# Performance work log

Measured on AMD Instinct MI355X. Metric: run time of the kernel, lower is better.

Reference implementation:

```python
import jax, jax.numpy as jnp
import numpy as np

B, S, C = 8, 512, 1024
H = 16
R = 32            # lora_rank
LORA_ALPHA = 1.0  # lora scaling (alpha=1)
HID = C           # mlp_ratio = 1


def setup_inputs() -> dict:
    key = jax.random.key(0)
    ks = jax.random.split(key, 20)
    g = lambda k, shp, s=0.02: jax.random.normal(k, shp, dtype=jnp.float32) * s
    inp = {
        "x": jax.random.normal(ks[0], (B, S, C), dtype=jnp.float32),
        "mask": jax.random.randint(ks[1], (B, 3 * S), 0, 2).astype(bool),
        # qkv: Linear(dim, 3*dim, bias=False), stored [in, out]
        "qkv_w": g(ks[2], (C, 3 * C)),
        "qkv_la": g(ks[3], (C, R)),
        "qkv_lb": g(ks[4], (R, 3 * C)),
        "proj_w": g(ks[5], (C, C)),
        "proj_b": jnp.zeros((C,), jnp.float32),
        "proj_la": g(ks[6], (C, R)),
        "proj_lb": g(ks[7], (R, C)),
        "fc1_w": g(ks[8], (C, HID)),
        "fc1_b": jnp.zeros((HID,), jnp.float32),
        "fc1_la": g(ks[9], (C, R)),
        "fc1_lb": g(ks[10], (R, HID)),
        "fc2_w": g(ks[11], (HID, C)),
        "fc2_b": jnp.zeros((C,), jnp.float32),
        "fc2_la": g(ks[12], (C, R)),
        "fc2_lb": g(ks[13], (R, C)),
    }
    return inp


def reference(x, mask, qkv_w, qkv_la, qkv_lb, proj_w, proj_b, proj_la, proj_lb,
              fc1_w, fc1_b, fc1_la, fc1_lb, fc2_w, fc2_b, fc2_la, fc2_lb):
    # cross_modality='a', mask_modality='a' (constants)
    b, s, c = x.shape
    hd = c // H
    scale = hd ** (-0.5)

    # fused QKV + LoRA low-rank update
    qkv = x @ qkv_w + ((x @ qkv_la) @ qkv_lb) * LORA_ALPHA      # [B,S,3C]
    qkv = qkv.reshape(b, s, 3, H, hd).transpose(2, 0, 3, 1, 4)  # [3,B,H,S,hd]
    q, k, v = qkv[0] * scale, qkv[1], qkv[2]

    # fp32 QK^T, modality 'a' mask slice, fill -inf, softmax, NaN->0
    attn = jnp.einsum('bhqd,bhkd->bhqk',
                      q.astype(jnp.float32), k.astype(jnp.float32))
    m = mask[:, :s]                                             # 'a' slice
    attn = jnp.where(m[:, None, None, :], attn, -jnp.inf)
    attn = jax.nn.softmax(attn, axis=-1).astype(x.dtype)
    attn = jnp.where(jnp.isnan(attn), jnp.zeros((), x.dtype), attn)

    xo = jnp.einsum('bhqk,bhkd->bhqd', attn, v)                 # [B,H,S,hd]
    xo = xo.transpose(0, 2, 1, 3).reshape(b, s, c)

    # MLP (with LoRA on both fc layers); torch nn.GELU default = exact erf
    h = xo @ fc1_w + fc1_b + ((xo @ fc1_la) @ fc1_lb) * LORA_ALPHA
    h = jax.nn.gelu(h, approximate=False)
    h = h @ fc2_w + fc2_b + ((h @ fc2_la) @ fc2_lb) * LORA_ALPHA
    xo = xo + h

    out = xo @ proj_w + proj_b + ((xo @ proj_la) @ proj_lb) * LORA_ALPHA
    return out
```

## Files before the change

### kernel.cpp

```cpp
#include <hip/hip_runtime.h>

typedef _Float16 f16;
typedef _Float16 f16x8 __attribute__((ext_vector_type(8)));
typedef _Float16 f16x4v __attribute__((ext_vector_type(4)));
typedef float f32x4 __attribute__((ext_vector_type(4)));

#define DEVINL __device__ __forceinline__

DEVINL void gload16(const void* g, void* l) {
  __builtin_amdgcn_global_load_lds(
      (const __attribute__((address_space(1))) void*)g,
      (__attribute__((address_space(3))) void*)l, 16, 0, 0);
}

__global__ __launch_bounds__(256) void weff3(
    const float* __restrict__ W, const float* __restrict__ la,
    const float* __restrict__ lb, f16* __restrict__ WT,
    int N, int K, int scaleCols)
{
  __shared__ float La[64][36];
  __shared__ f16 Ts[64][72];
  int t = threadIdx.x;
  int n0 = blockIdx.x * 64, k0 = blockIdx.y * 64;
  int w = t >> 6, nn = t & 63;
  #pragma unroll
  for (int i = 0; i < 8; ++i) {
    int idx = i * 256 + t;
    int row = idx >> 5, r = idx & 31;
    La[row][r] = la[(size_t)(k0 + row) * 32 + r];
  }
  float lbr[32];
  #pragma unroll
  for (int r = 0; r < 32; ++r) lbr[r] = lb[(size_t)r * N + n0 + nn];
  float scale = (n0 + nn < scaleCols) ? 0.125f : 1.0f;
  __syncthreads();
  float prev = 0.0f;
  #pragma unroll
  for (int i = 0; i < 16; ++i) {
    int k = w * 16 + i;
    float acc = W[(size_t)(k0 + k) * N + n0 + nn];
    #pragma unroll
    for (int rc = 0; rc < 8; ++rc) {
      float4 a4 = *(const float4*)&La[k][rc * 4];
      acc += a4.x * lbr[rc * 4] + a4.y * lbr[rc * 4 + 1] +
             a4.z * lbr[rc * 4 + 2] + a4.w * lbr[rc * 4 + 3];
    }
    acc *= scale;
    if (i & 1) {
      union { f16 h[2]; unsigned u; } pk;
      pk.h[0] = (f16)prev; pk.h[1] = (f16)acc;
      *(unsigned*)&Ts[nn][k - 1] = pk.u;
    } else prev = acc;
  }
  __syncthreads();
  #pragma unroll
  for (int it = 0; it < 2; ++it) {
    int id = it * 256 + t;
    int row = id >> 3, c8 = id & 7;
    f16x8 h = *(const f16x8*)&Ts[row][c8 * 8];
    *(f16x8*)(WT + (size_t)(n0 + row) * K + k0 + c8 * 8) = h;
  }
}

__global__ __launch_bounds__(256) void cvt_f32_f16(const float* __restrict__ in,
                                                   f16* __restrict__ out)
{
  int i = (blockIdx.x * 256 + threadIdx.x) * 4;
  float4 v = *(const float4*)(in + i);
  f16x4v o = {(f16)v.x, (f16)v.y, (f16)v.z, (f16)v.w};
  *(f16x4v*)(out + i) = o;
}

__global__ __launch_bounds__(256) void mask_canon(const unsigned char* __restrict__ m,
                                                  unsigned char* __restrict__ out)
{
  __shared__ int flag;
  if (threadIdx.x == 0) flag = 0;
  __syncthreads();
  int found = 0;
  for (int p = threadIdx.x; p < 12288; p += 256)
    if ((p & 3) && m[p]) found = 1;
  if (found) flag = 1;
  __syncthreads();
  int u8 = flag;
  const int* mi = (const int*)m;
  for (int idx = threadIdx.x; idx < 4096; idx += 256) {
    int b = idx >> 9, k = idx & 511;
    int v = u8 ? (int)m[b * 1536 + k] : mi[b * 1536 + k];
    out[idx] = (unsigned char)(v != 0);
  }
}

template <int EPI>
__global__ __launch_bounds__(256, 3) void gemmk(
    const f16* __restrict__ A, const f16* __restrict__ Bt,
    int M, int N, int K,
    const float* __restrict__ bias, const f16* __restrict__ resid,
    f16* __restrict__ outH, float* __restrict__ outF,
    f16* __restrict__ Qo, f16* __restrict__ Ko, f16* __restrict__ Vto)
{
  __shared__ __align__(16) f16 As[3][128 * 32];
  __shared__ __align__(16) f16 Bs[3][128 * 32];
  int tid = threadIdx.x, wid = tid >> 6, l = tid & 63;
  int lg = l >> 4, lr = l & 15;
  int nbx = gridDim.x;
  int flat = blockIdx.y * nbx + blockIdx.x;
  int xcd = flat & 7, idx = flat >> 3;
  int mc = nbx >> 3;
  int bm = (xcd * mc + idx % mc) * 128;
  int bn = (idx / mc) * 128;
  int wr = (wid >> 1) * 64, wc = (wid & 1) * 64;
  f32x4 acc[4][4] = {};

  int swz = ((l & 3) ^ ((l >> 3) & 3)) * 8;
  const f16* gA = A + (size_t)(bm + wid * 32 + (l >> 2)) * K + swz;
  const f16* gB = Bt + (size_t)(bn + wid * 32 + (l >> 2)) * K + swz;
  int lofs = wid * 32 * 32;
  int xr = (lr >> 1) & 3;

  f16* A0 = As[0]; f16* A1 = As[1]; f16* A2 = As[2];
  f16* B0 = Bs[0]; f16* B1 = Bs[1]; f16* B2 = Bs[2];

  #pragma unroll
  for (int ig = 0; ig < 2; ++ig) {
    gload16(gA + (size_t)(ig * 16) * K, A0 + lofs + ig * 16 * 32);
    gload16(gB + (size_t)(ig * 16) * K, B0 + lofs + ig * 16 * 32);
  }
  #pragma unroll
  for (int ig = 0; ig < 2; ++ig) {
    gload16(gA + (size_t)(ig * 16) * K + 32, A1 + lofs + ig * 16 * 32);
    gload16(gB + (size_t)(ig * 16) * K + 32, B1 + lofs + ig * 16 * 32);
  }

  int nt = K >> 5;
  for (int t = 0; t < nt; ++t) {
    if (t + 2 < nt) {
      int k2 = (t + 2) << 5;
      #pragma unroll
      for (int ig = 0; ig < 2; ++ig) {
        gload16(gA + (size_t)(ig * 16) * K + k2, A2 + lofs + ig * 16 * 32);
        gload16(gB + (size_t)(ig * 16) * K + k2, B2 + lofs + ig * 16 * 32);
      }
      asm volatile("s_waitcnt vmcnt(8)" ::: "memory");
    } else if (t + 2 == nt) {
      asm volatile("s_waitcnt vmcnt(4)" ::: "memory");
    } else {
      asm volatile("s_waitcnt vmcnt(0)" ::: "memory");
    }
    __builtin_amdgcn_s_barrier();

    f16x8 af[4], bf[4];
    #pragma unroll
    for (int i = 0; i < 4; ++i)
      af[i] = *(const f16x8*)(A0 + (wr + i * 16 + lr) * 32 + ((lg ^ xr) * 8));
    #pragma unroll
    for (int j = 0; j < 4; ++j)
      bf[j] = *(const f16x8*)(B0 + (wc + j * 16 + lr) * 32 + ((lg ^ xr) * 8));
    __builtin_amdgcn_s_setprio(1);
    #pragma unroll
    for (int i = 0; i < 4; ++i)
      #pragma unroll
      for (int j = 0; j < 4; ++j)
        acc[i][j] = __builtin_amdgcn_mfma_f32_16x16x32_f16(af[i], bf[j], acc[i][j], 0, 0, 0);
    __builtin_amdgcn_s_setprio(0);
    __builtin_amdgcn_sched_barrier(0);
    __builtin_amdgcn_s_barrier();

    f16* tA = A0; A0 = A1; A1 = A2; A2 = tA;
    f16* tB = B0; B0 = B1; B1 = B2; B2 = tB;
  }

  #pragma unroll
  for (int i = 0; i < 4; ++i) {
    #pragma unroll
    for (int j = 0; j < 4; ++j) {
      int n = bn + wc + j * 16 + lr;
      float bv = (EPI >= 1) ? bias[n] : 0.0f;
      #pragma unroll
      for (int r = 0; r < 4; ++r) {
        int m = bm + wr + i * 16 + lg * 4 + r;
        float v = acc[i][j][r];
        if (EPI == 0) {
          int bb = m >> 9, ss = m & 511;
          int which = n >> 10, c = n & 1023, hh = c >> 6, dd = c & 63;
          size_t base = (size_t)(bb * 16 + hh);
          if (which == 0)      Qo[(base * 512 + ss) * 64 + dd] = (f16)v;
          else if (which == 1) Ko[(base * 512 + ss) * 64 + dd] = (f16)v;
          else                 Vto[(base * 64 + dd) * 512 + ss] = (f16)v;
        } else if (EPI == 1) {
          v += bv;
          v = 0.5f * v * (1.0f + erff(v * 0.70710678118654752f));
          outH[(size_t)m * N + n] = (f16)v;
        } else if (EPI == 2) {
          v += bv + (float)resid[(size_t)m * N + n];
          outH[(size_t)m * N + n] = (f16)v;
        } else {
          outF[(size_t)m * N + n] = v + bv;
        }
      }
    }
  }
}

__global__ __launch_bounds__(256, 2) void attn_kernel(
    const f16* __restrict__ Q, const f16* __restrict__ Kc,
    const f16* __restrict__ Vt, const unsigned char* __restrict__ cmask,
    f16* __restrict__ XO)
{
  __shared__ __align__(16) f16 Ks[128 * 64];
  __shared__ __align__(16) f16 Vs[64 * 128];
  __shared__ __align__(16) f16 Ps[4 * 32 * 128];
  int tid = threadIdx.x, w = tid >> 6, l = tid & 63;
  int lg = l >> 4, lr = l & 15;
  int flat = blockIdx.y * 4 + blockIdx.x;
  flat = (flat & 7) * 64 + (flat >> 3);
  int qblk = flat & 3, bh = flat >> 2;
  int b = bh >> 4, h = bh & 15;
  const f16* Qg = Q + (size_t)bh * 512 * 64 + qblk * 128 * 64;
  const f16* Kg = Kc + (size_t)bh * 512 * 64;
  const f16* Vg = Vt + (size_t)bh * 64 * 512;
  const unsigned char* mb = cmask + b * 512;

  f16x8 qf[2][2];
  #pragma unroll
  for (int i = 0; i < 2; ++i)
    #pragma unroll
    for (int kc = 0; kc < 2; ++kc)
      qf[i][kc] = *(const f16x8*)(Qg + (size_t)(w * 32 + i * 16 + lr) * 64 + kc * 32 + lg * 8);

  f32x4 O[2][4] = {};
  float mrow[2][4], lrow[2][4];
  #pragma unroll
  for (int i = 0; i < 2; ++i)
    #pragma unroll
    for (int r = 0; r < 4; ++r) { mrow[i][r] = -1e30f; lrow[i][r] = 0.0f; }

  f16* Pw = Ps + w * 32 * 128;

  int kR = tid >> 3, kC = (tid & 7) * 8;
  int vR = tid >> 4, vC = (tid & 15) * 8;
  f16x8 kreg[4], vreg[4];
  #pragma unroll
  for (int i = 0; i < 4; ++i) {
    kreg[i] = *(const f16x8*)(Kg + (size_t)(i * 32 + kR) * 64 + kC);
    vreg[i] = *(const f16x8*)(Vg + (size_t)(i * 16 + vR) * 512 + vC);
  }

  for (int kt = 0; kt < 4; ++kt) {
    #pragma unroll
    for (int i = 0; i < 4; ++i) {
      int krow = i * 32 + kR;
      *(f16x8*)(Ks + krow * 64 + (((tid & 7) ^ (krow & 7)) * 8)) = kreg[i];
      int vrow = i * 16 + vR;
      *(f16x8*)(Vs + vrow * 128 + (((tid & 15) ^ (vrow & 7)) * 8)) = vreg[i];
    }
    __syncthreads();
    if (kt < 3) {
      #pragma unroll
      for (int i = 0; i < 4; ++i) {
        kreg[i] = *(const f16x8*)(Kg + (size_t)((kt + 1) * 128 + i * 32 + kR) * 64 + kC);
        vreg[i] = *(const f16x8*)(Vg + (size_t)(i * 16 + vR) * 512 + (kt + 1) * 128 + vC);
      }
    }

    int x = lr & 7;
    f32x4 sc[2][8] = {};
    __builtin_amdgcn_s_setprio(1);
    #pragma unroll
    for (int j = 0; j < 8; ++j) {
      const f16* krow = Ks + (j * 16 + lr) * 64;
      f16x8 kf0 = *(const f16x8*)(krow + ((lg ^ x) * 8));
      f16x8 kf1 = *(const f16x8*)(krow + (((4 + lg) ^ x) * 8));
      sc[0][j] = __builtin_amdgcn_mfma_f32_16x16x32_f16(qf[0][0], kf0, sc[0][j], 0, 0, 0);
      sc[0][j] = __builtin_amdgcn_mfma_f32_16x16x32_f16(qf[0][1], kf1, sc[0][j], 0, 0, 0);
      sc[1][j] = __builtin_amdgcn_mfma_f32_16x16x32_f16(qf[1][0], kf0, sc[1][j], 0, 0, 0);
      sc[1][j] = __builtin_amdgcn_mfma_f32_16x16x32_f16(qf[1][1], kf1, sc[1][j], 0, 0, 0);
    }
    __builtin_amdgcn_s_setprio(0);
    bool keep[8];
    #pragma unroll
    for (int j = 0; j < 8; ++j) keep[j] = mb[kt * 128 + j * 16 + lr] != 0;
    #pragma unroll
    for (int i = 0; i < 2; ++i)
      #pragma unroll
      for (int j = 0; j < 8; ++j)
        #pragma unroll
        for (int r = 0; r < 4; ++r)
          sc[i][j][r] = keep[j] ? sc[i][j][r] : -1e30f;

    #pragma unroll
    for (int i = 0; i < 2; ++i) {
      #pragma unroll
      for (int r = 0; r < 4; ++r) {
        float pm = sc[i][0][r];
        #pragma unroll
        for (int j = 1; j < 8; ++j) pm = fmaxf(pm, sc[i][j][r]);
        pm = fmaxf(pm, __shfl_xor(pm, 1));
        pm = fmaxf(pm, __shfl_xor(pm, 2));
        pm = fmaxf(pm, __shfl_xor(pm, 4));
        pm = fmaxf(pm, __shfl_xor(pm, 8));
        float mn = fmaxf(mrow[i][r], pm);
        float alpha = __expf(mrow[i][r] - mn);
        mrow[i][r] = mn;
        lrow[i][r] *= alpha;
        #pragma unroll
        for (int jd = 0; jd < 4; ++jd) O[i][jd][r] *= alpha;
      }
    }
    #pragma unroll
    for (int i = 0; i < 2; ++i) {
      float rs[4] = {0.f, 0.f, 0.f, 0.f};
      #pragma unroll
      for (int j = 0; j < 8; ++j)
        #pragma unroll
        for (int r = 0; r < 4; ++r) {
          float p = __expf(sc[i][j][r] - mrow[i][r]);
          rs[r] += p;
          int prow = i * 16 + lg * 4 + r;
          int pc = j * 16 + lr;
          Pw[prow * 128 + ((((pc >> 3) ^ (prow & 7)) << 3) | (pc & 7))] = (f16)p;
        }
      #pragma unroll
      for (int r = 0; r < 4; ++r) {
        float s = rs[r];
        s += __shfl_xor(s, 1); s += __shfl_xor(s, 2);
        s += __shfl_xor(s, 4); s += __shfl_xor(s, 8);
        lrow[i][r] += s;
      }
    }
    __builtin_amdgcn_s_setprio(1);
    #pragma unroll
    for (int kk = 0; kk < 4; ++kk) {
      int c0 = ((kk * 4 + lg) ^ x) * 8;
      f16x8 pa0 = *(const f16x8*)(Pw + lr * 128 + c0);
      f16x8 pa1 = *(const f16x8*)(Pw + (16 + lr) * 128 + c0);
      #pragma unroll
      for (int jd = 0; jd < 4; ++jd) {
        f16x8 vb = *(const f16x8*)(Vs + (jd * 16 + lr) * 128 + c0);
        O[0][jd] = __builtin_amdgcn_mfma_f32_16x16x32_f16(pa0, vb, O[0][jd], 0, 0, 0);
        O[1][jd] = __builtin_amdgcn_mfma_f32_16x16x32_f16(pa1, vb, O[1][jd], 0, 0, 0);
      }
    }
    __builtin_amdgcn_s_setprio(0);
    __syncthreads();
  }

  #pragma unroll
  for (int i = 0; i < 2; ++i)
    #pragma unroll
    for (int r = 0; r < 4; ++r) {
      int q = qblk * 128 + w * 32 + i * 16 + lg * 4 + r;
      float inv = 1.0f / lrow[i][r];
      #pragma unroll
      for (int jd = 0; jd < 4; ++jd) {
        int c = h * 64 + jd * 16 + lr;
        XO[((size_t)b * 512 + q) * 1024 + c] = (f16)(O[i][jd][r] * inv);
      }
    }
}

extern "C" void kernel_launch(void* const* d_in, const int* in_sizes, int n_in,
                              void* d_out, int out_size, void* d_ws, size_t ws_size,
                              hipStream_t stream)
{
  (void)in_sizes; (void)n_in; (void)out_size; (void)ws_size;
  const float* x            = (const float*)d_in[0];
  const unsigned char* mask = (const unsigned char*)d_in[1];
  const float* qkv_w   = (const float*)d_in[2];
  const float* qkv_la  = (const float*)d_in[3];
  const float* qkv_lb  = (const float*)d_in[4];
  const float* proj_w  = (const float*)d_in[5];
  const float* proj_b  = (const float*)d_in[6];
  const float* proj_la = (const float*)d_in[7];
  const float* proj_lb = (const float*)d_in[8];
  const float* fc1_w   = (const float*)d_in[9];
  const float* fc1_b   = (const float*)d_in[10];
  const float* fc1_la  = (const float*)d_in[11];
  const float* fc1_lb  = (const float*)d_in[12];
  const float* fc2_w   = (const float*)d_in[13];
  const float* fc2_b   = (const float*)d_in[14];
  const float* fc2_la  = (const float*)d_in[15];
  const float* fc2_lb  = (const float*)d_in[16];
  float* out = (float*)d_out;

  f16* p = (f16*)d_ws;
  f16* WqkvT = p; p += 3072 * 1024;
  f16* W1T   = p; p += 1024 * 1024;
  f16* W2T   = p; p += 1024 * 1024;
  f16* WpT   = p; p += 1024 * 1024;
  f16* Xh    = p; p += 4096 * 1024;
  f16* Qb    = p; p += 128 * 512 * 64;
  f16* Kb    = p; p += 128 * 512 * 64;
  f16* Vt    = p; p += 128 * 64 * 512;
  f16* XO    = p; p += 4096 * 1024;
  unsigned char* cmask = (unsigned char*)p;
  f16* Hb  = Qb;
  f16* XO2 = Xh;

  weff3<<<dim3(48, 16), 256, 0, stream>>>(qkv_w, qkv_la, qkv_lb, WqkvT, 3072, 1024, 1024);
  weff3<<<dim3(16, 16), 256, 0, stream>>>(fc1_w, fc1_la, fc1_lb, W1T, 1024, 1024, 0);
  weff3<<<dim3(16, 16), 256, 0, stream>>>(fc2_w, fc2_la, fc2_lb, W2T, 1024, 1024, 0);
  weff3<<<dim3(16, 16), 256, 0, stream>>>(proj_w, proj_la, proj_lb, WpT, 1024, 1024, 0);
  cvt_f32_f16<<<4096, 256, 0, stream>>>(x, Xh);
  mask_canon<<<1, 256, 0, stream>>>(mask, cmask);

  gemmk<0><<<dim3(32, 24), 256, 0, stream>>>(Xh, WqkvT, 4096, 3072, 1024,
      nullptr, nullptr, nullptr, nullptr, Qb, Kb, Vt);
  attn_kernel<<<dim3(4, 128), 256, 0, stream>>>(Qb, Kb, Vt, cmask, XO);
  gemmk<1><<<dim3(32, 8), 256, 0, stream>>>(XO, W1T, 4096, 1024, 1024,
      fc1_b, nullptr, Hb, nullptr, nullptr, nullptr, nullptr);
  gemmk<2><<<dim3(32, 8), 256, 0, stream>>>(Hb, W2T, 4096, 1024, 1024,
      fc2_b, XO, XO2, nullptr, nullptr, nullptr, nullptr);
  gemmk<3><<<dim3(32, 8), 256, 0, stream>>>(XO2, WpT, 4096, 1024, 1024,
      proj_b, nullptr, nullptr, out, nullptr, nullptr, nullptr);
}
```

Baseline: 293.4 us.

## Add 64x64-tile GEMM for the 1024-wide layers and shrink attention P buffer

New measurement: 283.1 us. 1.04x faster.

```diff
diff --git a/kernel.cpp b/kernel.cpp
--- a/kernel.cpp
+++ b/kernel.cpp
@@ -202,14 +202,118 @@
   }
 }
 
-__global__ __launch_bounds__(256, 2) void attn_kernel(
+template <int EPI>
+__global__ __launch_bounds__(256, 4) void gemm64(
+    const f16* __restrict__ A, const f16* __restrict__ Bt,
+    int M, int N, int K,
+    const float* __restrict__ bias, const f16* __restrict__ resid,
+    f16* __restrict__ outH, float* __restrict__ outF)
+{
+  __shared__ __align__(16) f16 As[2][64 * 64];
+  __shared__ __align__(16) f16 Bs[2][64 * 64];
+  int tid = threadIdx.x, wid = tid >> 6, l = tid & 63;
+  int lg = l >> 4, lr = l & 15;
+  int nbx = gridDim.x;
+  int flat = blockIdx.y * nbx + blockIdx.x;
+  int xcd = flat & 7, idx = flat >> 3;
+  int mc = nbx >> 3;
+  int bm = (xcd * mc + idx % mc) * 64;
+  int bn = (idx / mc) * 64;
+  int wr = (wid >> 1) * 32, wc = (wid & 1) * 32;
+  f32x4 acc[2][2] = {};
+
+  int srow = l >> 3;
+  int swz = ((l & 7) ^ srow) * 8;
+  const f16* gA = A + (size_t)(bm + wid * 16 + srow) * K + swz;
+  const f16* gB = Bt + (size_t)(bn + wid * 16 + srow) * K + swz;
+  int lofs = wid * 16 * 64;
+  int xr = lr & 7;
+
+  #pragma unroll
+  for (int ig = 0; ig < 2; ++ig) {
+    gload16(gA + (size_t)(ig * 8) * K, As[0] + lofs + ig * 8 * 64);
+    gload16(gB + (size_t)(ig * 8) * K, Bs[0] + lofs + ig * 8 * 64);
+  }
+  #pragma unroll
+  for (int ig = 0; ig < 2; ++ig) {
+    gload16(gA + (size_t)(ig * 8) * K + 64, As[1] + lofs + ig * 8 * 64);
+    gload16(gB + (size_t)(ig * 8) * K + 64, Bs[1] + lofs + ig * 8 * 64);
+  }
+
+  int nt = K >> 6;
+  for (int t = 0; t < nt; ++t) {
+    if (t < nt - 1) asm volatile("s_waitcnt vmcnt(4)" ::: "memory");
+    else            asm volatile("s_waitcnt vmcnt(0)" ::: "memory");
+    __builtin_amdgcn_s_barrier();
+    __builtin_amdgcn_sched_barrier(0);
+
+    const f16* Ac = As[t & 1];
+    const f16* Bc = Bs[t & 1];
+    f16x8 af[2][2], bf[2][2];
+    #pragma unroll
+    for (int kk = 0; kk < 2; ++kk) {
+      #pragma unroll
+      for (int i = 0; i < 2; ++i)
+        af[kk][i] = *(const f16x8*)(Ac + (wr + i * 16 + lr) * 64 + (((kk * 4 + lg) ^ xr) * 8));
+      #pragma unroll
+      for (int j = 0; j < 2; ++j)
+        bf[kk][j] = *(const f16x8*)(Bc + (wc + j * 16 + lr) * 64 + (((kk * 4 + lg) ^ xr) * 8));
+    }
+    __builtin_amdgcn_s_setprio(1);
+    #pragma unroll
+    for (int kk = 0; kk < 2; ++kk)
+      #pragma unroll
+      for (int i = 0; i < 2; ++i)
+        #pragma unroll
+        for (int j = 0; j < 2; ++j)
+          acc[i][j] = __builtin_amdgcn_mfma_f32_16x16x32_f16(af[kk][i], bf[kk][j], acc[i][j], 0, 0, 0);
+    __builtin_amdgcn_s_setprio(0);
+    __builtin_amdgcn_sched_barrier(0);
+    __builtin_amdgcn_s_barrier();
+    __builtin_amdgcn_sched_barrier(0);
+    if (t + 2 < nt) {
+      int k2 = (t + 2) << 6;
+      #pragma unroll
+      for (int ig = 0; ig < 2; ++ig) {
+        gload16(gA + (size_t)(ig * 8) * K + k2, As[t & 1] + lofs + ig * 8 * 64);
+        gload16(gB + (size_t)(ig * 8) * K + k2, Bs[t & 1] + lofs + ig * 8 * 64);
+      }
+    }
+  }
+
+  #pragma unroll
+  for (int i = 0; i < 2; ++i) {
+    #pragma unroll
+    for (int j = 0; j < 2; ++j) {
+      int n = bn + wc + j * 16 + lr;
+      float bv = bias[n];
+      #pragma unroll
+      for (int r = 0; r < 4; ++r) {
+        int m = bm + wr + i * 16 + lg * 4 + r;
+        float v = acc[i][j][r];
+        if (EPI == 1) {
+          v += bv;
+          v = 0.5f * v * (1.0f + erff(v * 0.70710678118654752f));
+          outH[(size_t)m * N + n] = (f16)v;
+        } else if (EPI == 2) {
+          v += bv + (float)resid[(size_t)m * N + n];
+          outH[(size_t)m * N + n] = (f16)v;
+        } else {
+          outF[(size_t)m * N + n] = v + bv;
+        }
+      }
+    }
+  }
+}
+
+__global__ __launch_bounds__(256) void attn_kernel(
     const f16* __restrict__ Q, const f16* __restrict__ Kc,
     const f16* __restrict__ Vt, const unsigned char* __restrict__ cmask,
     f16* __restrict__ XO)
 {
   __shared__ __align__(16) f16 Ks[128 * 64];
   __shared__ __align__(16) f16 Vs[64 * 128];
-  __shared__ __align__(16) f16 Ps[4 * 32 * 128];
+  __shared__ __align__(16) f16 Ps[4 * 16 * 128];
   int tid = threadIdx.x, w = tid >> 6, l = tid & 63;
   int lg = l >> 4, lr = l & 15;
   int flat = blockIdx.y * 4 + blockIdx.x;
@@ -235,7 +339,7 @@
     #pragma unroll
     for (int r = 0; r < 4; ++r) { mrow[i][r] = -1e30f; lrow[i][r] = 0.0f; }
 
-  f16* Pw = Ps + w * 32 * 128;
+  f16* Pw = Ps + w * 16 * 128;
 
   int kR = tid >> 3, kC = (tid & 7) * 8;
   int vR = tid >> 4, vC = (tid & 15) * 8;
@@ -316,7 +420,7 @@
         for (int r = 0; r < 4; ++r) {
           float p = __expf(sc[i][j][r] - mrow[i][r]);
           rs[r] += p;
-          int prow = i * 16 + lg * 4 + r;
+          int prow = lg * 4 + r;
           int pc = j * 16 + lr;
           Pw[prow * 128 + ((((pc >> 3) ^ (prow & 7)) << 3) | (pc & 7))] = (f16)p;
         }
@@ -327,21 +431,19 @@
         s += __shfl_xor(s, 4); s += __shfl_xor(s, 8);
         lrow[i][r] += s;
       }
-    }
-    __builtin_amdgcn_s_setprio(1);
-    #pragma unroll
-    for (int kk = 0; kk < 4; ++kk) {
-      int c0 = ((kk * 4 + lg) ^ x) * 8;
-      f16x8 pa0 = *(const f16x8*)(Pw + lr * 128 + c0);
-      f16x8 pa1 = *(const f16x8*)(Pw + (16 + lr) * 128 + c0);
-      #pragma unroll
-      for (int jd = 0; jd < 4; ++jd) {
-        f16x8 vb = *(const f16x8*)(Vs + (jd * 16 + lr) * 128 + c0);
-        O[0][jd] = __builtin_amdgcn_mfma_f32_16x16x32_f16(pa0, vb, O[0][jd], 0, 0, 0);
-        O[1][jd] = __builtin_amdgcn_mfma_f32_16x16x32_f16(pa1, vb, O[1][jd], 0, 0, 0);
-      }
-    }
-    __builtin_amdgcn_s_setprio(0);
+      __builtin_amdgcn_s_setprio(1);
+      #pragma unroll
+      for (int kk = 0; kk < 4; ++kk) {
+        int c0 = ((kk * 4 + lg) ^ x) * 8;
+        f16x8 pa = *(const f16x8*)(Pw + lr * 128 + c0);
+        #pragma unroll
+        for (int jd = 0; jd < 4; ++jd) {
+          f16x8 vb = *(const f16x8*)(Vs + (jd * 16 + lr) * 128 + c0);
+          O[i][jd] = __builtin_amdgcn_mfma_f32_16x16x32_f16(pa, vb, O[i][jd], 0, 0, 0);
+        }
+      }
+      __builtin_amdgcn_s_setprio(0);
+    }
     __syncthreads();
   }
 
@@ -407,10 +509,10 @@
   gemmk<0><<<dim3(32, 24), 256, 0, stream>>>(Xh, WqkvT, 4096, 3072, 1024,
       nullptr, nullptr, nullptr, nullptr, Qb, Kb, Vt);
   attn_kernel<<<dim3(4, 128), 256, 0, stream>>>(Qb, Kb, Vt, cmask, XO);
-  gemmk<1><<<dim3(32, 8), 256, 0, stream>>>(XO, W1T, 4096, 1024, 1024,
-      fc1_b, nullptr, Hb, nullptr, nullptr, nullptr, nullptr);
-  gemmk<2><<<dim3(32, 8), 256, 0, stream>>>(Hb, W2T, 4096, 1024, 1024,
-      fc2_b, XO, XO2, nullptr, nullptr, nullptr, nullptr);
-  gemmk<3><<<dim3(32, 8), 256, 0, stream>>>(XO2, WpT, 4096, 1024, 1024,
-      proj_b, nullptr, nullptr, out, nullptr, nullptr, nullptr);
-}
+  gemm64<1><<<dim3(64, 16), 256, 0, stream>>>(XO, W1T, 4096, 1024, 1024,
+      fc1_b, nullptr, Hb, nullptr);
+  gemm64<2><<<dim3(64, 16), 256, 0, stream>>>(Hb, W2T, 4096, 1024, 1024,
+      fc2_b, XO, XO2, nullptr);
+  gemm64<3><<<dim3(64, 16), 256, 0, stream>>>(XO2, WpT, 4096, 1024, 1024,
+      proj_b, nullptr, nullptr, out);
+}
```
